# Kernel tuning notes

Hardware: AMD Instinct MI355X
Metric: run time of the kernel (lower is better)

## Reference

```python
import jax, jax.numpy as jnp
import numpy as np

GRID_SIZE = 300


def setup_inputs() -> dict:
    key = jax.random.key(0)
    k1, k2 = jax.random.split(key)
    N, input_dim, out_dim = 2048, 256, 256
    x = jax.random.normal(k1, (N, input_dim), dtype=jnp.float32)
    scale = 1.0 / (np.sqrt(input_dim) * np.sqrt(GRID_SIZE))
    coeffs = jax.random.normal(k2, (2, out_dim, input_dim, GRID_SIZE), dtype=jnp.float32) * scale
    bias = jnp.zeros((1, out_dim), dtype=jnp.float32)
    return {"x": x, "coeffs": coeffs, "bias": bias}


def reference(x, coeffs, bias):
    # x: [N, I]; coeffs: [2, J, I, K]; bias: [1, J]
    grid_size = coeffs.shape[-1]
    k = jnp.arange(1, grid_size + 1, dtype=x.dtype)            # [K]
    ang = x[:, :, None] * k                                    # [N, I, K]
    c = jnp.cos(ang)
    s = jnp.sin(ang)
    # einsum('dbik,djik->bj') with d=2 split into cos/sin parts
    y = jnp.einsum('bik,jik->bj', c, coeffs[0]) + jnp.einsum('bik,jik->bj', s, coeffs[1])
    y = y + bias
    return y
```

## Files before the change

kernel.cpp:

```cpp
#include <hip/hip_runtime.h>
#include <stdint.h>

#define NB 2048
#define NI 256
#define NJ 256
#define GK 300
#define KPAD 320
#define KK_PER_I (2*KPAD)
#define NKC (NI*KK_PER_I/32)
#define SPLITK 16
#define BM 128
#define BN 128

typedef __bf16 bf16x8 __attribute__((ext_vector_type(8)));
typedef __bf16 bf16x2 __attribute__((ext_vector_type(2)));
typedef float  f32x4  __attribute__((ext_vector_type(4)));
typedef __attribute__((address_space(1))) const unsigned int gu32;
typedef __attribute__((address_space(3))) unsigned int lu32;

__device__ __forceinline__ void sincos2pi(float ang, float& c, float& s) {
  float r = ang * 0.15915494309189535f;
  r = r - floorf(r);
  c = __builtin_amdgcn_cosf(r);
  s = __builtin_amdgcn_sinf(r);
}

__global__ __launch_bounds__(256) void convert_b(const float* __restrict__ coeffs,
                                                 unsigned int* __restrict__ bw) {
  const unsigned int tid = blockIdx.x * 256u + threadIdx.x;
  const unsigned int jjpair = tid & 3u;
  const unsigned int n      = (tid >> 2) & 15u;
  const unsigned int q      = (tid >> 6) & 3u;
  const unsigned int jt     = (tid >> 8) & 15u;
  const unsigned int kc     = tid >> 12;
  const unsigned int kk = kc * 32u + q * 8u + jjpair * 2u;
  const unsigned int i  = kk / KK_PER_I;
  const unsigned int k  = (kk % KK_PER_I) >> 1;
  const unsigned int j  = jt * 16u + n;
  unsigned int val = 0u;
  if (k < GK) {
    float c0 = coeffs[(j * NI + i) * GK + k];
    float c1 = coeffs[((NJ + j) * NI + i) * GK + k];
    bf16x2 p; p.x = (__bf16)c0; p.y = (__bf16)c1;
    val = __builtin_bit_cast(unsigned int, p);
  }
  bw[tid] = val;
}

__global__ __launch_bounds__(256) void init_out(const float* __restrict__ bias,
                                                float* __restrict__ out) {
  const int tid = blockIdx.x * 256 + threadIdx.x;
  float4 b = ((const float4*)bias)[tid & 63];
  ((float4*)out)[tid] = b;
}

__global__ __launch_bounds__(256, 2) void fkan_gemm(const float* __restrict__ x,
                                                    const unsigned int* __restrict__ bw,
                                                    float* __restrict__ out) {
  __shared__ uint4 lds4[2048];
  char* lds = (char*)lds4;

  const int bid = blockIdx.x;
  const int mt = bid & 15;
  const int nt = (bid >> 4) & 1;
  const int s  = bid >> 5;
  const int m0 = mt * BM;

  const int t    = (int)threadIdx.x;
  const int lane = t & 63;
  const int wave = t >> 6;

  const int gn  = t & 15;
  const int gmt = (t >> 4) & 7;
  const int gkc = t >> 7;
  const int grow = gmt * 16 + gn;
  const float* xptr = x + (m0 + grow) * NI;
  const unsigned int abase = (unsigned int)((gkc * 8 + gmt) * 1024 + gn * 16);

  const int wr = wave >> 1;
  const int wc = wave & 1;

  f32x4 acc[4][4];
  #pragma unroll
  for (int mm = 0; mm < 4; mm++)
    #pragma unroll
    for (int nn = 0; nn < 4; nn++)
      acc[mm][nn] = (f32x4){0.f, 0.f, 0.f, 0.f};

  const int kc0 = s * (NKC / SPLITK);

  #pragma unroll 1
  for (int ii = 0; ii < 16; ii++) {
    const int i = s * 16 + ii;
    const float xv = xptr[i];
    float c1, s1, c32, s32, ccur, scur;
    sincos2pi(xv, c1, s1);
    sincos2pi(32.f * xv, c32, s32);
    sincos2pi(xv * (float)(gkc * 16 + 1), ccur, scur);

    #pragma unroll 1
    for (int t10 = 0; t10 < 10; t10++) {
      __syncthreads();

      float cc = ccur, ss = scur;
      #pragma unroll
      for (int q = 0; q < 4; q++) {
        uint4 w;
        #pragma unroll
        for (int p = 0; p < 4; p++) {
          bf16x2 pk; pk.x = (__bf16)cc; pk.y = (__bf16)ss;
          ((unsigned int*)&w)[p] = __builtin_bit_cast(unsigned int, pk);
          float nc = cc * c1 - ss * s1;
          ss = ss * c1 + cc * s1;
          cc = nc;
        }
        *(uint4*)(lds + abase + q * 256) = w;
      }
      {
        float nc = ccur * c32 - scur * s32;
        scur = scur * c32 + ccur * s32;
        ccur = nc;
      }

      const int kc = kc0 + ii * (KK_PER_I / 32) + t10 * 2;
      #pragma unroll
      for (int q2 = 0; q2 < 4; q2++) {
        const int idx = wave * 4 + q2;
        const int kcoff = idx >> 3;
        const int jtoff = idx & 7;
        const unsigned int* src = bw + ((((kc + kcoff) * 16) + nt * 8 + jtoff) << 8)
                                     + lane * 4;
        unsigned int* dst = (unsigned int*)(lds + 16384 + idx * 1024);
        __builtin_amdgcn_global_load_lds((gu32*)src, (lu32*)dst, 16, 0, 0);
      }

      __syncthreads();

      #pragma unroll
      for (int ks = 0; ks < 2; ks++) {
        bf16x8 af[4], bfr[4];
        #pragma unroll
        for (int mm = 0; mm < 4; mm++)
          af[mm] = *(bf16x8*)(lds + (ks * 8 + wr * 4 + mm) * 1024 + lane * 16);
        #pragma unroll
        for (int nn = 0; nn < 4; nn++)
          bfr[nn] = *(bf16x8*)(lds + 16384 + (ks * 8 + wc * 4 + nn) * 1024 + lane * 16);
        #pragma unroll
        for (int mm = 0; mm < 4; mm++)
          #pragma unroll
          for (int nn = 0; nn < 4; nn++)
            acc[mm][nn] = __builtin_amdgcn_mfma_f32_16x16x32_bf16(
                af[mm], bfr[nn], acc[mm][nn], 0, 0, 0);
      }
    }
  }

  const int r0 = m0 + wr * 64 + ((lane >> 4) << 2);
  const int c0 = nt * BN + wc * 64 + (lane & 15);
  #pragma unroll
  for (int mm = 0; mm < 4; mm++)
    #pragma unroll
    for (int nn = 0; nn < 4; nn++)
      #pragma unroll
      for (int r = 0; r < 4; r++)
        atomicAdd(&out[(r0 + mm * 16 + r) * NJ + c0 + nn * 16], acc[mm][nn][r]);
}

extern "C" void kernel_launch(void* const* d_in, const int* in_sizes, int n_in,
                              void* d_out, int out_size, void* d_ws, size_t ws_size,
                              hipStream_t stream) {
  const float* x      = (const float*)d_in[0];
  const float* coeffs = (const float*)d_in[1];
  const float* bias   = (const float*)d_in[2];
  float* out = (float*)d_out;
  unsigned int* bw = (unsigned int*)d_ws;

  convert_b<<<dim3(NKC * 16), dim3(256), 0, stream>>>(coeffs, bw);
  init_out<<<dim3(NB * NJ / 4 / 256), dim3(256), 0, stream>>>(bias, out);
  fkan_gemm<<<dim3(16 * 2 * SPLITK), dim3(256), 0, stream>>>(x, bw, out);
}
```

Before: 465.5 us.

## Vectorize coefficient bf16 conversion and double split-K factor

Rewrites the coefficient-conversion kernel so each thread reads contiguous float4 runs along the grid dimension and writes packed uint4 stores. This replaces the scattered per-element reads of the earlier version. Split-K also doubles from 16 to 32, so the GEMM launches 1024 blocks with half the input features each. That gives better CU occupancy in exchange for twice as many atomic adds into the output.

```diff
diff --git a/kernel.cpp b/kernel.cpp
--- a/kernel.cpp
+++ b/kernel.cpp
@@ -8,7 +8,8 @@
 #define KPAD 320
 #define KK_PER_I (2*KPAD)
 #define NKC (NI*KK_PER_I/32)
-#define SPLITK 16
+#define SPLITK 32
+#define II_PER_S (NI / SPLITK)
 #define BM 128
 #define BN 128
 
@@ -27,24 +28,37 @@
 
 __global__ __launch_bounds__(256) void convert_b(const float* __restrict__ coeffs,
                                                  unsigned int* __restrict__ bw) {
-  const unsigned int tid = blockIdx.x * 256u + threadIdx.x;
-  const unsigned int jjpair = tid & 3u;
-  const unsigned int n      = (tid >> 2) & 15u;
-  const unsigned int q      = (tid >> 6) & 3u;
-  const unsigned int jt     = (tid >> 8) & 15u;
-  const unsigned int kc     = tid >> 12;
-  const unsigned int kk = kc * 32u + q * 8u + jjpair * 2u;
-  const unsigned int i  = kk / KK_PER_I;
-  const unsigned int k  = (kk % KK_PER_I) >> 1;
-  const unsigned int j  = jt * 16u + n;
-  unsigned int val = 0u;
-  if (k < GK) {
-    float c0 = coeffs[(j * NI + i) * GK + k];
-    float c1 = coeffs[((NJ + j) * NI + i) * GK + k];
-    bf16x2 p; p.x = (__bf16)c0; p.y = (__bf16)c1;
-    val = __builtin_bit_cast(unsigned int, p);
+  const int bid = blockIdx.x;
+  const int i  = bid >> 4;
+  const int jt = bid & 15;
+  const int t  = (int)threadIdx.x;
+  const int n  = t & 15;
+  const int gl = t >> 4;
+  const int j  = jt * 16 + n;
+
+  const float4* r0 = (const float4*)(coeffs + (size_t)(j * NI + i) * GK);
+  const float4* r1 = (const float4*)(coeffs + (size_t)((NJ + j) * NI + i) * GK);
+
+  #pragma unroll
+  for (int p = 0; p < 5; p++) {
+    const int g = p * 16 + gl;
+    uint4 w = {0u, 0u, 0u, 0u};
+    if (g < GK / 4) {
+      float4 a = r0[g];
+      float4 b = r1[g];
+      bf16x2 p0; p0.x = (__bf16)a.x; p0.y = (__bf16)b.x;
+      bf16x2 p1; p1.x = (__bf16)a.y; p1.y = (__bf16)b.y;
+      bf16x2 p2; p2.x = (__bf16)a.z; p2.y = (__bf16)b.z;
+      bf16x2 p3; p3.x = (__bf16)a.w; p3.y = (__bf16)b.w;
+      w.x = __builtin_bit_cast(unsigned int, p0);
+      w.y = __builtin_bit_cast(unsigned int, p1);
+      w.z = __builtin_bit_cast(unsigned int, p2);
+      w.w = __builtin_bit_cast(unsigned int, p3);
+    }
+    const int kc = i * 20 + (g >> 2);
+    const unsigned int idx = ((unsigned int)(kc * 16 + jt) << 8) + ((g & 3) << 6) + (n << 2);
+    *(uint4*)(bw + idx) = w;
   }
-  bw[tid] = val;
 }
 
 __global__ __launch_bounds__(256) void init_out(const float* __restrict__ bias,
@@ -90,8 +104,8 @@
   const int kc0 = s * (NKC / SPLITK);
 
   #pragma unroll 1
-  for (int ii = 0; ii < 16; ii++) {
-    const int i = s * 16 + ii;
+  for (int ii = 0; ii < II_PER_S; ii++) {
+    const int i = s * II_PER_S + ii;
     const float xv = xptr[i];
     float c1, s1, c32, s32, ccur, scur;
     sincos2pi(xv, c1, s1);
@@ -175,7 +189,7 @@
   float* out = (float*)d_out;
   unsigned int* bw = (unsigned int*)d_ws;
 
-  convert_b<<<dim3(NKC * 16), dim3(256), 0, stream>>>(coeffs, bw);
+  convert_b<<<dim3(NI * 16), dim3(256), 0, stream>>>(coeffs, bw);
   init_out<<<dim3(NB * NJ / 4 / 256), dim3(256), 0, stream>>>(bias, out);
   fkan_gemm<<<dim3(16 * 2 * SPLITK), dim3(256), 0, stream>>>(x, bw, out);
 }
```

Result: no change. 460.0 us (-1.2%).
